# Kernel tuning notes

Hardware: AMD Instinct MI355X
Metric: run time of the kernel (lower is better)

Reference implementation:

```python
import jax, jax.numpy as jnp
import numpy as np

# Production-scale dims: ViT patch attention on a 32x32 patch grid
B, L, F = 16, 1024, 512      # batch, seq (=NX*NY patches), model dim
H, D = 8, 64                 # heads, head_dim (F = H*D)
NX, NY = 32, 32              # patch grid; Toeplitz table size 4*NX*NY = 4096


def setup_inputs() -> dict:
    key = jax.random.key(0)
    ks = jax.random.split(key, 12)
    w = lambda k, shp: jax.random.normal(k, shp, jnp.float32) * 0.02
    return {
        "inputs_q": jax.random.normal(ks[0], (B, L, F), jnp.float32),
        "inputs_kv": jax.random.normal(ks[1], (B, L, F), jnp.float32),
        "Wq": w(ks[2], (F, H * D)), "bq": jnp.zeros((H * D,), jnp.float32),
        "Wk": w(ks[3], (F, H * D)), "bk": jnp.zeros((H * D,), jnp.float32),
        "Wv": w(ks[4], (F, H * D)), "bv": jnp.zeros((H * D,), jnp.float32),
        "Wo": w(ks[5], (H * D, F)), "bo": jnp.zeros((F,), jnp.float32),
        "toeplitz": w(ks[6], (H, 4 * NX * NY)),
    }


def _rel_index():
    # 2D relative-position (Toeplitz) index: patch p -> (x, y) on NX x NY grid.
    coords = jnp.arange(L)
    xi, yi = coords // NY, coords % NY
    dx = xi[:, None] - xi[None, :] + NX          # in [1, 2*NX-1]
    dy = yi[:, None] - yi[None, :] + NY          # in [1, 2*NY-1]
    return dx * (2 * NY) + dy                    # [L, L] indices into 4*NX*NY table


def reference(inputs_q, inputs_kv, Wq, bq, Wk, bk, Wv, bv, Wo, bo, toeplitz):
    q = (inputs_q @ Wq + bq).reshape(B, L, H, D)
    k = (inputs_kv @ Wk + bk).reshape(B, L, H, D)
    v = (inputs_kv @ Wv + bv).reshape(B, L, H, D)
    bias = toeplitz[:, _rel_index()]             # [H, L, L] Toeplitz relative bias
    scale = 1.0 / jnp.sqrt(jnp.float32(D))
    scores = jnp.einsum("bqhd,bkhd->bhqk", q, k) * scale + bias  # [B,H,L,L]
    attn = jax.nn.softmax(scores, axis=-1)
    x = jnp.einsum("bhqk,bkhd->bqhd", attn, v).reshape(B, L, H * D)
    out = x @ Wo + bo
    return out.reshape(B, L, H, D)               # matches torch forward's final reshape
```

## Files before the change

### kernel.cpp

```cpp
#include <hip/hip_runtime.h>
#include <hip/hip_bf16.h>

#define B_  16
#define L_  1024
#define F_  512
#define H_  8
#define D_  64
#define M_  (B_ * L_)
#define HD_ 512

typedef __bf16 bf16x8 __attribute__((ext_vector_type(8)));
typedef __bf16 bf16x4 __attribute__((ext_vector_type(4)));
typedef float  f32x4  __attribute__((ext_vector_type(4)));

__device__ __forceinline__ void gl_lds16(const void* g, void* l) {
  __builtin_amdgcn_global_load_lds(
      (const __attribute__((address_space(1))) unsigned int*)g,
      (__attribute__((address_space(3))) unsigned int*)l, 16, 0, 0);
}

__global__ __launch_bounds__(256) void wt_kernel(
    const float* __restrict__ Wq, const float* __restrict__ Wk,
    const float* __restrict__ Wv, const float* __restrict__ Wo,
    __bf16* __restrict__ Wt_all)
{
  const float* W = (blockIdx.z == 0) ? Wq : (blockIdx.z == 1) ? Wk
                 : (blockIdx.z == 2) ? Wv : Wo;
  __bf16* Wt = Wt_all + (size_t)blockIdx.z * (512 * 512);
  __shared__ float s[32][33];
  const int t = threadIdx.x;
  const int r = t >> 5, c = t & 31;
  const int k0 = blockIdx.x * 32, n0 = blockIdx.y * 32;
#pragma unroll
  for (int i = 0; i < 4; ++i)
    s[r + i * 8][c] = W[(size_t)(k0 + r + i * 8) * 512 + n0 + c];
  __syncthreads();
#pragma unroll
  for (int i = 0; i < 4; ++i)
    Wt[(size_t)(n0 + r + i * 8) * 512 + k0 + c] = (__bf16)s[c][r + i * 8];
}

__global__ __launch_bounds__(256) void gemm_proj_kernel(
    const float* __restrict__ Xq, const float* __restrict__ Xkv,
    const __bf16* __restrict__ Wt_all,
    const float* __restrict__ bq, const float* __restrict__ bk_,
    const float* __restrict__ bv_,
    __bf16* __restrict__ qd, __bf16* __restrict__ kd, __bf16* __restrict__ vd)
{
  const int seg = blockIdx.y >> 2;
  const float* X = (seg == 0) ? Xq : Xkv;
  const __bf16* Wt = Wt_all + (size_t)seg * 262144;
  const float* bias = (seg == 0) ? bq : (seg == 1) ? bk_ : bv_;
  __bf16* dst = (seg == 0) ? qd : (seg == 1) ? kd : vd;
  const int mode = seg;

  __shared__ __align__(16) __bf16 As[4][128][8];
  __shared__ __align__(16) __bf16 Bs[4][128][8];
  const int t = threadIdx.x;
  const int m0 = blockIdx.x * 128, n0 = (blockIdx.y & 3) * 128;
  const int lane = t & 63, w = t >> 6;
  const int ml = lane & 15, quad = lane >> 4;
  const int wm = w & 1, wn = w >> 1;

  f32x4 acc[4][4];
#pragma unroll
  for (int i = 0; i < 4; ++i)
#pragma unroll
    for (int j = 0; j < 4; ++j) acc[i][j] = (f32x4){0.f, 0.f, 0.f, 0.f};

  for (int k0 = 0; k0 < 512; k0 += 32) {
    __syncthreads();
#pragma unroll
    for (int i = 0; i < 2; ++i) {
      int slot = (w + i * 4) * 64 + lane;
      int ko = slot >> 7, row = slot & 127;
      gl_lds16(&Wt[(size_t)(n0 + row) * 512 + k0 + ko * 8], &Bs[ko][row][0]);
    }
#pragma unroll
    for (int i = 0; i < 2; ++i) {
      int slot = t + i * 256;
      int ko = slot & 3, row = slot >> 2;
      const float* src = X + (size_t)(m0 + row) * 512 + k0 + ko * 8;
      float4 f0 = *(const float4*)src;
      float4 f1 = *(const float4*)(src + 4);
      bf16x8 v;
      v[0] = (__bf16)f0.x; v[1] = (__bf16)f0.y; v[2] = (__bf16)f0.z; v[3] = (__bf16)f0.w;
      v[4] = (__bf16)f1.x; v[5] = (__bf16)f1.y; v[6] = (__bf16)f1.z; v[7] = (__bf16)f1.w;
      *(bf16x8*)&As[ko][row][0] = v;
    }
    __syncthreads();
    bf16x8 a[4], b[4];
#pragma unroll
    for (int mt = 0; mt < 4; ++mt)
      a[mt] = *(const bf16x8*)&As[quad][wm * 64 + mt * 16 + ml][0];
#pragma unroll
    for (int nt = 0; nt < 4; ++nt)
      b[nt] = *(const bf16x8*)&Bs[quad][wn * 64 + nt * 16 + ml][0];
#pragma unroll
    for (int mt = 0; mt < 4; ++mt)
#pragma unroll
      for (int nt = 0; nt < 4; ++nt)
        acc[mt][nt] =
            __builtin_amdgcn_mfma_f32_16x16x32_bf16(a[mt], b[nt], acc[mt][nt], 0, 0, 0);
  }

#pragma unroll
  for (int nt = 0; nt < 4; ++nt) {
    int col = n0 + wn * 64 + nt * 16 + ml;
    float bv = bias[col];
    int h = col >> 6, d = col & 63;
#pragma unroll
    for (int mt = 0; mt < 4; ++mt) {
      int row0 = m0 + wm * 64 + mt * 16 + quad * 4;
      int bz = row0 >> 10;
      int l0 = row0 & 1023;
      if (mode == 2) {
        bf16x4 pk;
#pragma unroll
        for (int r = 0; r < 4; ++r) pk[r] = (__bf16)(acc[mt][nt][r] + bv);
        size_t idx = ((size_t)(bz * H_ + h) * D_ + d) * L_ + l0;
        *(bf16x4*)&dst[idx] = pk;
      } else {
        size_t base = ((size_t)(bz * H_ + h) * L_ + l0) * D_ + d;
#pragma unroll
        for (int r = 0; r < 4; ++r)
          dst[base + (size_t)r * D_] = (__bf16)(acc[mt][nt][r] + bv);
      }
    }
  }
}

__global__ __launch_bounds__(256) void attn_kernel(
    const __bf16* __restrict__ qg,
    const __bf16* __restrict__ kg,
    const __bf16* __restrict__ vg,
    const float* __restrict__ toep_g,
    __bf16* __restrict__ xg)
{
  __shared__ float toep[4096];
  __shared__ __align__(16) __bf16 Ks[2][64][64];
  __shared__ __align__(16) __bf16 Vs[2][64][64];
  __shared__ __align__(16) __bf16 Ps[4][2][8][16][8];

  const int t = threadIdx.x;
  const int n = blockIdx.x;
  const int bh = ((n >> 6) << 3) | (n & 7);
  const int q0 = ((n >> 3) & 7) * 128;
  const int h = bh & 7;
  const int lane = t & 63, w = t >> 6;
  const int ml = lane & 15, quad = lane >> 4;
  const int lo3 = lane >> 3;
  const int kop = lane & 7;

  const size_t qkbase = (size_t)bh * (L_ * D_);
  const size_t vbase  = (size_t)bh * (D_ * L_);

  {
    const float4* src = (const float4*)(toep_g + (size_t)h * 4096);
    float4* dl = (float4*)toep;
    for (int i = t; i < 1024; i += 256) dl[i] = src[i];
  }

#pragma unroll
  for (int i = 0; i < 2; ++i) {
    int j = w * 2 + i;
    int row = j * 8 + lo3;
    int ko = kop ^ lo3;
    gl_lds16(&kg[qkbase + (size_t)row * D_ + ko * 8], &Ks[0][row][kop * 8]);
    gl_lds16(&vg[vbase + (size_t)row * L_ + ko * 8], &Vs[0][row][kop * 8]);
  }

  bf16x8 qf[2][2];
#pragma unroll
  for (int qn = 0; qn < 2; ++qn) {
    const __bf16* qp =
        qg + qkbase + (size_t)(q0 + w * 32 + qn * 16 + ml) * D_ + quad * 8;
    qf[qn][0] = *(const bf16x8*)qp;
    qf[qn][1] = *(const bf16x8*)(qp + 32);
  }

  const int dxq = ((q0 >> 5) + w);

  float lpart[2] = {0.f, 0.f};
  f32x4 o[2][4];
#pragma unroll
  for (int qn = 0; qn < 2; ++qn)
#pragma unroll
    for (int dt = 0; dt < 4; ++dt) o[qn][dt] = (f32x4){0.f, 0.f, 0.f, 0.f};

  __syncthreads();

  int cur = 0;
  for (int k0 = 0; k0 < L_; k0 += 64) {
    if (k0 + 64 < L_) {
      int nb = cur ^ 1;
#pragma unroll
      for (int i = 0; i < 2; ++i) {
        int j = w * 2 + i;
        int row = j * 8 + lo3;
        int ko = kop ^ lo3;
        gl_lds16(&kg[qkbase + (size_t)(k0 + 64 + row) * D_ + ko * 8],
                 &Ks[nb][row][kop * 8]);
        gl_lds16(&vg[vbase + (size_t)row * L_ + k0 + 64 + ko * 8],
                 &Vs[nb][row][kop * 8]);
      }
    }

    f32x4 st[2][4];
#pragma unroll
    for (int nt = 0; nt < 4; ++nt) {
      bf16x8 kf0 = *(const bf16x8*)&Ks[cur][nt * 16 + ml][(quad ^ (ml & 7)) * 8];
      bf16x8 kf1 = *(const bf16x8*)&Ks[cur][nt * 16 + ml][((4 + quad) ^ (ml & 7)) * 8];
#pragma unroll
      for (int qn = 0; qn < 2; ++qn) {
        f32x4 z = (f32x4){0.f, 0.f, 0.f, 0.f};
        z = __builtin_amdgcn_mfma_f32_16x16x32_bf16(kf0, qf[qn][0], z, 0, 0, 0);
        st[qn][nt] =
            __builtin_amdgcn_mfma_f32_16x16x32_bf16(kf1, qf[qn][1], z, 0, 0, 0);
      }
    }

#pragma unroll
    for (int qn = 0; qn < 2; ++qn) {
      int dyq = qn * 16 + ml;
#pragma unroll
      for (int nt = 0; nt < 4; ++nt) {
        int kx = (k0 >> 5) + (nt >> 1);
        int base = (dxq - kx + 32) * 64 + (dyq - ((nt & 1) * 16 + quad * 4) + 32);
        float p[4];
#pragma unroll
        for (int r = 0; r < 4; ++r)
          p[r] = __expf(fmaf(st[qn][nt][r], 0.125f, toep[base - r]));
        lpart[qn] += (p[0] + p[1]) + (p[2] + p[3]);
        bf16x4 pk;
#pragma unroll
        for (int r = 0; r < 4; ++r) pk[r] = (__bf16)p[r];
        *(bf16x4*)&Ps[w][qn][nt * 2 + (quad >> 1)][ml][(quad & 1) * 4] = pk;
      }
    }

#pragma unroll
    for (int kb = 0; kb < 2; ++kb) {
      bf16x8 pf0 = *(const bf16x8*)&Ps[w][0][kb * 4 + quad][ml][0];
      bf16x8 pf1 = *(const bf16x8*)&Ps[w][1][kb * 4 + quad][ml][0];
#pragma unroll
      for (int dt = 0; dt < 4; ++dt) {
        bf16x8 vf = *(const bf16x8*)&Vs[cur][dt * 16 + ml]
                                       [((kb * 4 + quad) ^ (ml & 7)) * 8];
        o[0][dt] = __builtin_amdgcn_mfma_f32_16x16x32_bf16(pf0, vf, o[0][dt], 0, 0, 0);
        o[1][dt] = __builtin_amdgcn_mfma_f32_16x16x32_bf16(pf1, vf, o[1][dt], 0, 0, 0);
      }
    }

    __syncthreads();
    cur ^= 1;
  }

#pragma unroll
  for (int qn = 0; qn < 2; ++qn) {
    lpart[qn] += __shfl_xor(lpart[qn], 16);
    lpart[qn] += __shfl_xor(lpart[qn], 32);
  }
  float linv[2][4];
#pragma unroll
  for (int qn = 0; qn < 2; ++qn)
#pragma unroll
    for (int r = 0; r < 4; ++r)
      linv[qn][r] = 1.0f / __shfl(lpart[qn], quad * 16 + quad * 4 + r);

#pragma unroll
  for (int qn = 0; qn < 2; ++qn)
#pragma unroll
    for (int dt = 0; dt < 4; ++dt)
#pragma unroll
      for (int r = 0; r < 4; ++r) {
        int row = q0 + w * 32 + qn * 16 + quad * 4 + r;
        xg[((size_t)(bh >> 3) * L_ + row) * 512 + h * 64 + dt * 16 + ml] =
            (__bf16)(o[qn][dt][r] * linv[qn][r]);
      }
}

__global__ __launch_bounds__(256) void gemm_out_kernel(
    const __bf16* __restrict__ Xb,
    const __bf16* __restrict__ Wt,
    const float* __restrict__ bo,
    float* __restrict__ out)
{
  __shared__ __align__(16) __bf16 As[4][128][8];
  __shared__ __align__(16) __bf16 Bs[4][128][8];
  const int t = threadIdx.x;
  const int m0 = blockIdx.x * 128, n0 = blockIdx.y * 128;
  const int lane = t & 63, w = t >> 6;
  const int ml = lane & 15, quad = lane >> 4;
  const int wm = w & 1, wn = w >> 1;

  f32x4 acc[4][4];
#pragma unroll
  for (int i = 0; i < 4; ++i)
#pragma unroll
    for (int j = 0; j < 4; ++j) acc[i][j] = (f32x4){0.f, 0.f, 0.f, 0.f};

  for (int k0 = 0; k0 < 512; k0 += 32) {
    __syncthreads();
#pragma unroll
    for (int i = 0; i < 2; ++i) {
      int slot = (w + i * 4) * 64 + lane;
      int ko = slot >> 7, row = slot & 127;
      gl_lds16(&Xb[(size_t)(m0 + row) * 512 + k0 + ko * 8], &As[ko][row][0]);
      gl_lds16(&Wt[(size_t)(n0 + row) * 512 + k0 + ko * 8], &Bs[ko][row][0]);
    }
    __syncthreads();
    bf16x8 a[4], b[4];
#pragma unroll
    for (int mt = 0; mt < 4; ++mt)
      a[mt] = *(const bf16x8*)&As[quad][wm * 64 + mt * 16 + ml][0];
#pragma unroll
    for (int nt = 0; nt < 4; ++nt)
      b[nt] = *(const bf16x8*)&Bs[quad][wn * 64 + nt * 16 + ml][0];
#pragma unroll
    for (int mt = 0; mt < 4; ++mt)
#pragma unroll
      for (int nt = 0; nt < 4; ++nt)
        acc[mt][nt] =
            __builtin_amdgcn_mfma_f32_16x16x32_bf16(a[mt], b[nt], acc[mt][nt], 0, 0, 0);
  }

#pragma unroll
  for (int nt = 0; nt < 4; ++nt) {
    int col = n0 + wn * 64 + nt * 16 + ml;
    float bv = bo[col];
#pragma unroll
    for (int mt = 0; mt < 4; ++mt) {
      int row0 = m0 + wm * 64 + mt * 16 + quad * 4;
#pragma unroll
      for (int r = 0; r < 4; ++r)
        out[(size_t)(row0 + r) * 512 + col] = acc[mt][nt][r] + bv;
    }
  }
}

extern "C" void kernel_launch(void* const* d_in, const int* in_sizes, int n_in,
                              void* d_out, int out_size, void* d_ws, size_t ws_size,
                              hipStream_t stream) {
  const float* inputs_q  = (const float*)d_in[0];
  const float* inputs_kv = (const float*)d_in[1];
  const float* Wq = (const float*)d_in[2];
  const float* bq = (const float*)d_in[3];
  const float* Wk = (const float*)d_in[4];
  const float* bk = (const float*)d_in[5];
  const float* Wv = (const float*)d_in[6];
  const float* bv = (const float*)d_in[7];
  const float* Wo = (const float*)d_in[8];
  const float* bo = (const float*)d_in[9];
  const float* toep = (const float*)d_in[10];
  float* out = (float*)d_out;

  char* ws = (char*)d_ws;
  __bf16* qb = (__bf16*)(ws);
  __bf16* kb = (__bf16*)(ws + 16777216);
  __bf16* vb = (__bf16*)(ws + 33554432);
  __bf16* xb = (__bf16*)(ws + 50331648);
  __bf16* Wt = (__bf16*)(ws + 67108864);

  wt_kernel<<<dim3(16, 16, 4), 256, 0, stream>>>(Wq, Wk, Wv, Wo, Wt);
  gemm_proj_kernel<<<dim3(128, 12), 256, 0, stream>>>(
      inputs_q, inputs_kv, Wt, bq, bk, bv, qb, kb, vb);
  attn_kernel<<<dim3(1024), 256, 0, stream>>>(qb, kb, vb, toep, xb);
  gemm_out_kernel<<<dim3(128, 4), 256, 0, stream>>>(xb, Wt + 3 * 262144, bo, out);
}
```

Measured before the change: 259.9 us.

## Keep P in registers and double per-block query tile in attention

The attention kernel now covers 256 query rows per block (64 per wave) and launches 512 blocks instead of 1024. Each K/V tile loaded into LDS is therefore reused across twice as many queries. The LDS round trip for the probability matrix is removed by feeding the QK^T accumulator layout straight into 16x16x16 bf16 MFMAs as the A operand, with V read in matching 4-element fragments. This raises register pressure (launch bounds set to 3 blocks) and uses the smaller-K MFMA, so fewer blocks may hurt occupancy and load balance.

```diff
diff --git a/kernel.cpp b/kernel.cpp
--- a/kernel.cpp
+++ b/kernel.cpp
@@ -11,6 +11,7 @@
 
 typedef __bf16 bf16x8 __attribute__((ext_vector_type(8)));
 typedef __bf16 bf16x4 __attribute__((ext_vector_type(4)));
+typedef short  s16x4  __attribute__((ext_vector_type(4)));
 typedef float  f32x4  __attribute__((ext_vector_type(4)));
 
 __device__ __forceinline__ void gl_lds16(const void* g, void* l) {
@@ -130,7 +131,7 @@
   }
 }
 
-__global__ __launch_bounds__(256) void attn_kernel(
+__global__ __launch_bounds__(256, 3) void attn_kernel(
     const __bf16* __restrict__ qg,
     const __bf16* __restrict__ kg,
     const __bf16* __restrict__ vg,
@@ -140,12 +141,11 @@
   __shared__ float toep[4096];
   __shared__ __align__(16) __bf16 Ks[2][64][64];
   __shared__ __align__(16) __bf16 Vs[2][64][64];
-  __shared__ __align__(16) __bf16 Ps[4][2][8][16][8];
 
   const int t = threadIdx.x;
   const int n = blockIdx.x;
-  const int bh = ((n >> 6) << 3) | (n & 7);
-  const int q0 = ((n >> 3) & 7) * 128;
+  const int bh = ((n >> 5) << 3) | (n & 7);
+  const int q0 = ((n >> 3) & 3) * 256;
   const int h = bh & 7;
   const int lane = t & 63, w = t >> 6;
   const int ml = lane & 15, quad = lane >> 4;
@@ -163,28 +163,25 @@
 
 #pragma unroll
   for (int i = 0; i < 2; ++i) {
-    int j = w * 2 + i;
-    int row = j * 8 + lo3;
+    int row = (w * 2 + i) * 8 + lo3;
     int ko = kop ^ lo3;
     gl_lds16(&kg[qkbase + (size_t)row * D_ + ko * 8], &Ks[0][row][kop * 8]);
     gl_lds16(&vg[vbase + (size_t)row * L_ + ko * 8], &Vs[0][row][kop * 8]);
   }
 
-  bf16x8 qf[2][2];
-#pragma unroll
-  for (int qn = 0; qn < 2; ++qn) {
+  bf16x8 qf[4][2];
+#pragma unroll
+  for (int qn = 0; qn < 4; ++qn) {
     const __bf16* qp =
-        qg + qkbase + (size_t)(q0 + w * 32 + qn * 16 + ml) * D_ + quad * 8;
+        qg + qkbase + (size_t)(q0 + w * 64 + qn * 16 + ml) * D_ + quad * 8;
     qf[qn][0] = *(const bf16x8*)qp;
     qf[qn][1] = *(const bf16x8*)(qp + 32);
   }
 
-  const int dxq = ((q0 >> 5) + w);
-
-  float lpart[2] = {0.f, 0.f};
-  f32x4 o[2][4];
-#pragma unroll
-  for (int qn = 0; qn < 2; ++qn)
+  float lpart[4] = {0.f, 0.f, 0.f, 0.f};
+  f32x4 o[4][4];
+#pragma unroll
+  for (int qn = 0; qn < 4; ++qn)
 #pragma unroll
     for (int dt = 0; dt < 4; ++dt) o[qn][dt] = (f32x4){0.f, 0.f, 0.f, 0.f};
 
@@ -196,8 +193,7 @@
       int nb = cur ^ 1;
 #pragma unroll
       for (int i = 0; i < 2; ++i) {
-        int j = w * 2 + i;
-        int row = j * 8 + lo3;
+        int row = (w * 2 + i) * 8 + lo3;
         int ko = kop ^ lo3;
         gl_lds16(&kg[qkbase + (size_t)(k0 + 64 + row) * D_ + ko * 8],
                  &Ks[nb][row][kop * 8]);
@@ -206,49 +202,45 @@
       }
     }
 
-    f32x4 st[2][4];
 #pragma unroll
     for (int nt = 0; nt < 4; ++nt) {
       bf16x8 kf0 = *(const bf16x8*)&Ks[cur][nt * 16 + ml][(quad ^ (ml & 7)) * 8];
-      bf16x8 kf1 = *(const bf16x8*)&Ks[cur][nt * 16 + ml][((4 + quad) ^ (ml & 7)) * 8];
-#pragma unroll
-      for (int qn = 0; qn < 2; ++qn) {
+      bf16x8 kf1 =
+          *(const bf16x8*)&Ks[cur][nt * 16 + ml][((4 + quad) ^ (ml & 7)) * 8];
+      int kx = (k0 >> 5) + (nt >> 1);
+
+      s16x4 pfrag[4];
+#pragma unroll
+      for (int qn = 0; qn < 4; ++qn) {
         f32x4 z = (f32x4){0.f, 0.f, 0.f, 0.f};
         z = __builtin_amdgcn_mfma_f32_16x16x32_bf16(kf0, qf[qn][0], z, 0, 0, 0);
-        st[qn][nt] =
-            __builtin_amdgcn_mfma_f32_16x16x32_bf16(kf1, qf[qn][1], z, 0, 0, 0);
-      }
-    }
-
-#pragma unroll
-    for (int qn = 0; qn < 2; ++qn) {
-      int dyq = qn * 16 + ml;
-#pragma unroll
-      for (int nt = 0; nt < 4; ++nt) {
-        int kx = (k0 >> 5) + (nt >> 1);
-        int base = (dxq - kx + 32) * 64 + (dyq - ((nt & 1) * 16 + quad * 4) + 32);
+        z = __builtin_amdgcn_mfma_f32_16x16x32_bf16(kf1, qf[qn][1], z, 0, 0, 0);
+
+        int qb = w * 64 + qn * 16;
+        int base = (((q0 + qb) >> 5) - kx + 32) * 64 +
+                   ((qb & 31) + ml - ((nt & 1) * 16 + quad * 4) + 32);
         float p[4];
 #pragma unroll
         for (int r = 0; r < 4; ++r)
-          p[r] = __expf(fmaf(st[qn][nt][r], 0.125f, toep[base - r]));
+          p[r] = __expf(fmaf(z[r], 0.125f, toep[base - r]));
         lpart[qn] += (p[0] + p[1]) + (p[2] + p[3]);
         bf16x4 pk;
 #pragma unroll
         for (int r = 0; r < 4; ++r) pk[r] = (__bf16)p[r];
-        *(bf16x4*)&Ps[w][qn][nt * 2 + (quad >> 1)][ml][(quad & 1) * 4] = pk;
-      }
-    }
-
-#pragma unroll
-    for (int kb = 0; kb < 2; ++kb) {
-      bf16x8 pf0 = *(const bf16x8*)&Ps[w][0][kb * 4 + quad][ml][0];
-      bf16x8 pf1 = *(const bf16x8*)&Ps[w][1][kb * 4 + quad][ml][0];
+        pfrag[qn] = __builtin_bit_cast(s16x4, pk);
+      }
+
 #pragma unroll
       for (int dt = 0; dt < 4; ++dt) {
-        bf16x8 vf = *(const bf16x8*)&Vs[cur][dt * 16 + ml]
-                                       [((kb * 4 + quad) ^ (ml & 7)) * 8];
-        o[0][dt] = __builtin_amdgcn_mfma_f32_16x16x32_bf16(pf0, vf, o[0][dt], 0, 0, 0);
-        o[1][dt] = __builtin_amdgcn_mfma_f32_16x16x32_bf16(pf1, vf, o[1][dt], 0, 0, 0);
+        int row = dt * 16 + ml;
+        int gc = nt * 2 + (quad >> 1);
+        bf16x4 vfr = *(const bf16x4*)
+            &Vs[cur][row][((gc ^ (row & 7)) * 8) + (quad & 1) * 4];
+        s16x4 vfs = __builtin_bit_cast(s16x4, vfr);
+#pragma unroll
+        for (int qn = 0; qn < 4; ++qn)
+          o[qn][dt] = __builtin_amdgcn_mfma_f32_16x16x16bf16_1k(
+              pfrag[qn], vfs, o[qn][dt], 0, 0, 0);
       }
     }
 
@@ -257,24 +249,24 @@
   }
 
 #pragma unroll
-  for (int qn = 0; qn < 2; ++qn) {
+  for (int qn = 0; qn < 4; ++qn) {
     lpart[qn] += __shfl_xor(lpart[qn], 16);
     lpart[qn] += __shfl_xor(lpart[qn], 32);
   }
-  float linv[2][4];
-#pragma unroll
-  for (int qn = 0; qn < 2; ++qn)
+  float linv[4][4];
+#pragma unroll
+  for (int qn = 0; qn < 4; ++qn)
 #pragma unroll
     for (int r = 0; r < 4; ++r)
       linv[qn][r] = 1.0f / __shfl(lpart[qn], quad * 16 + quad * 4 + r);
 
 #pragma unroll
-  for (int qn = 0; qn < 2; ++qn)
+  for (int qn = 0; qn < 4; ++qn)
 #pragma unroll
     for (int dt = 0; dt < 4; ++dt)
 #pragma unroll
       for (int r = 0; r < 4; ++r) {
-        int row = q0 + w * 32 + qn * 16 + quad * 4 + r;
+        int row = q0 + w * 64 + qn * 16 + quad * 4 + r;
         xg[((size_t)(bh >> 3) * L_ + row) * 512 + h * 64 + dt * 16 + ml] =
             (__bf16)(o[qn][dt][r] * linv[qn][r]);
       }
@@ -365,6 +357,6 @@
   wt_kernel<<<dim3(16, 16, 4), 256, 0, stream>>>(Wq, Wk, Wv, Wo, Wt);
   gemm_proj_kernel<<<dim3(128, 12), 256, 0, stream>>>(
       inputs_q, inputs_kv, Wt, bq, bk, bv, qb, kb, vb);
-  attn_kernel<<<dim3(1024), 256, 0, stream>>>(qb, kb, vb, toep, xb);
+  attn_kernel<<<dim3(512), 256, 0, stream>>>(qb, kb, vb, toep, xb);
   gemm_out_kernel<<<dim3(128, 4), 256, 0, stream>>>(xb, Wt + 3 * 262144, bo, out);
 }
```

Result: slower. 408.8 us (+57.3%).
